# Optimization experiments

Measured on AMD Instinct MI355X. Metric: run time of the kernel, lower is better.

Reference implementation:

```python
import jax, jax.numpy as jnp
import numpy as np

EPS = 1e-5
N_NODES = 50000


def batchnorm(x, gamma, beta):
    # training-mode BatchNorm1d: batch mean, biased variance
    mean = jnp.mean(x, axis=0)
    var = jnp.mean(jnp.square(x - mean), axis=0)
    return (x - mean) * jax.lax.rsqrt(var + EPS) * gamma + beta


def setup_inputs() -> dict:
    key = jax.random.key(0)
    ks = jax.random.split(key, 8)
    N, E, D_IN, D_H, D_OUT = N_NODES, 800000, 128, 128, 128
    feat = jax.random.normal(ks[0], (N, D_IN), dtype=jnp.float32)
    w = jax.random.uniform(ks[1], (E,), dtype=jnp.float32)
    # xavier_uniform with relu gain for Q and W
    gain = float(np.sqrt(2.0))
    bq = gain * np.sqrt(6.0 / (D_IN + D_H))
    bw = gain * np.sqrt(6.0 / (D_IN + D_H + D_OUT))
    Q_w = jax.random.uniform(ks[2], (D_H, D_IN), minval=-bq, maxval=bq, dtype=jnp.float32)
    W_w = jax.random.uniform(ks[3], (D_OUT, D_IN + D_H), minval=-bw, maxval=bw, dtype=jnp.float32)
    Q_b = jnp.zeros((D_H,), jnp.float32)
    W_b = jnp.zeros((D_OUT,), jnp.float32)
    gamma2 = jnp.ones((D_OUT,), jnp.float32)
    beta2 = jnp.zeros((D_OUT,), jnp.float32)
    src = jax.random.randint(ks[4], (E,), 0, N, dtype=jnp.int32)
    dst = jax.random.randint(ks[5], (E,), 0, N, dtype=jnp.int32)
    return {"feat": feat, "w": w, "Q_w": Q_w, "Q_b": Q_b, "W_w": W_w,
            "W_b": W_b, "gamma2": gamma2, "beta2": beta2, "src": src, "dst": dst}


def reference(feat, w, Q_w, Q_b, W_w, W_b, gamma2, beta2, src, dst):
    N = feat.shape[0]
    # h = dropout(bnorm_two(relu(Q(feat))))  (dropout=0 -> identity; source reuses bnorm_two)
    h = batchnorm(jax.nn.relu(feat @ Q_w.T + Q_b), gamma2, beta2)  # [N, H]
    # weighted neighbor mean: sum_e w_e * h[src_e] scattered to dst, / sum_e w_e
    num = jax.ops.segment_sum(w[:, None] * h[src], dst, num_segments=N)  # [N, H]
    den = jax.ops.segment_sum(w, dst, num_segments=N)  # [N]
    has_msg = den[:, None] != 0
    agg = jnp.where(has_msg, num / jnp.where(has_msg, den[:, None], 1.0), h)
    rst = jnp.concatenate([feat, agg], axis=1) @ W_w.T + W_b  # [N, OUT]
    rst = batchnorm(jax.nn.relu(rst), gamma2, beta2)
    denom = jnp.linalg.norm(rst, axis=1, keepdims=True)
    return rst / jnp.where(denom == 0, 1.0, denom)
```

## Files before the change

### kernel.cpp

```cpp
#include <hip/hip_runtime.h>
#include <stdint.h>


#define BN_EPS 1e-5f
#define NSLOT 32

typedef __attribute__((ext_vector_type(8))) short bf16x8;
typedef __attribute__((ext_vector_type(4))) float f32x4;

static __device__ __forceinline__ unsigned short f2bf(float f) {
    uint32_t u = __builtin_bit_cast(uint32_t, f);
    u += 0x7fffu + ((u >> 16) & 1u);
    return (unsigned short)(u >> 16);
}
static __device__ __forceinline__ float bf_lo(uint32_t u) {
    return __builtin_bit_cast(float, u << 16);
}
static __device__ __forceinline__ float bf_hi(uint32_t u) {
    return __builtin_bit_cast(float, u & 0xffff0000u);
}

__global__ __launch_bounds__(256) void k_pre(
    const float* __restrict__ feat, unsigned short* __restrict__ featb, int nf,
    const int* __restrict__ dst, int* __restrict__ cnt, int E, int CB)
{
    if ((int)blockIdx.x < CB) {
        int i = (blockIdx.x * 256 + threadIdx.x) * 4;
        if (i + 3 < nf) {
            float4 v = *(const float4*)(feat + i);
            ushort4 o;
            o.x = f2bf(v.x); o.y = f2bf(v.y); o.z = f2bf(v.z); o.w = f2bf(v.w);
            *(ushort4*)(featb + i) = o;
        } else {
            for (int j = i; j < nf; ++j) featb[j] = f2bf(feat[j]);
        }
    } else {
        int e = (blockIdx.x - CB) * 256 + threadIdx.x;
        if (e < E) atomicAdd(&cnt[dst[e]], 1);
    }
}

__global__ __launch_bounds__(1024) void k_scan_part(
    const int* __restrict__ cnt, int* __restrict__ offs,
    int* __restrict__ bsum)
{
    __shared__ int wsum[16];
    const int tid = threadIdx.x, lane = tid & 63, wv = tid >> 6;
    const int i = blockIdx.x * 4096 + tid * 4;
    int4 v = *(const int4*)(cnt + i);
    int s = v.x + v.y + v.z + v.w;
    int incl = s;
#pragma unroll
    for (int o = 1; o < 64; o <<= 1) {
        int t = __shfl_up(incl, o, 64);
        if (lane >= o) incl += t;
    }
    if (lane == 63) wsum[wv] = incl;
    __syncthreads();
    if (wv == 0 && lane < 16) {
        int t = wsum[lane];
        int ss = t;
#pragma unroll
        for (int o = 1; o < 16; o <<= 1) {
            int u = __shfl_up(ss, o, 64);
            if (lane >= o) ss += u;
        }
        wsum[lane] = ss - t;
        if (lane == 15 && bsum) bsum[blockIdx.x] = ss;
    }
    __syncthreads();
    int e0 = wsum[wv] + incl - s;
    int4 o;
    o.x = e0; o.y = e0 + v.x; o.z = o.y + v.y; o.w = o.z + v.z;
    *(int4*)(offs + i) = o;
}

__global__ __launch_bounds__(1024) void k_scan_fix(
    int* __restrict__ offs, const int* __restrict__ bsum,
    int* __restrict__ gcur, int N, int E)
{
    __shared__ int pre_s;
    const int tid = threadIdx.x;
    if (tid == 0) {
        int p = 0;
        for (int j = 0; j < (int)blockIdx.x; ++j) p += bsum[j];
        pre_s = p;
    }
    __syncthreads();
    const int pre = pre_s;
    const int i = blockIdx.x * 4096 + tid * 4;
    int4 v = *(const int4*)(offs + i);
    v.x += pre; v.y += pre; v.z += pre; v.w += pre;
    if (i + 3 < N) {
        *(int4*)(offs + i) = v;
    } else {
        int vv[4] = {v.x, v.y, v.z, v.w};
        for (int j = 0; j < 4; ++j) {
            int idx = i + j;
            if (idx < N) offs[idx] = vv[j];
            else if (idx == N) offs[idx] = E;
        }
    }
    if ((tid & 127) == 0 && i < N) gcur[i >> 9] = v.x;
}

template<int K>
__global__ __launch_bounds__(256) void gemm_bn(
    const unsigned short* __restrict__ A_lo,
    const unsigned short* __restrict__ A_hi,
    const float* __restrict__ B,
    const float* __restrict__ bias,
    float* __restrict__ Y,
    double* __restrict__ sum, double* __restrict__ sumsq, int N)
{
    constexpr int SA = 72;
    __shared__ unsigned short As[64 * SA];
    __shared__ unsigned short Bs[128 * SA];
    __shared__ float bsum_s[128], bsq_s[128];

    const int tid  = threadIdx.x;
    const int lane = tid & 63;
    const int wv   = tid >> 6;
    const int wr   = wv >> 1;
    const int wc   = wv & 1;
    const int m15  = lane & 15;
    const int quad = lane >> 4;
    const int r0   = blockIdx.x * 64;

    if (tid < 128) { bsum_s[tid] = 0.f; bsq_s[tid] = 0.f; }

    f32x4 acc[2][4];
#pragma unroll
    for (int rt = 0; rt < 2; ++rt)
#pragma unroll
        for (int ct = 0; ct < 4; ++ct)
            acc[rt][ct] = (f32x4){0.f, 0.f, 0.f, 0.f};

    for (int kc = 0; kc < K; kc += 64) {
        const unsigned short* Ap = (kc < 128) ? A_lo : A_hi;
        const int koff = kc & 127;
#pragma unroll
        for (int i = 0; i < 2; ++i) {
            int idx = i * 256 + tid;
            int row = idx >> 3, seg = idx & 7;
            int gr  = r0 + row; if (gr >= N) gr = N - 1;
            uint4 v = *(const uint4*)(Ap + (size_t)gr * 128 + koff + seg * 8);
            *(uint4*)(As + row * SA + seg * 8) = v;
        }
#pragma unroll
        for (int i = 0; i < 8; ++i) {
            int idx = i * 256 + tid;
            int row = idx >> 4, seg = idx & 15;
            float4 v = *(const float4*)(B + (size_t)row * K + kc + seg * 4);
            ushort4 o;
            o.x = f2bf(v.x); o.y = f2bf(v.y); o.z = f2bf(v.z); o.w = f2bf(v.w);
            *(ushort4*)(Bs + row * SA + seg * 4) = o;
        }
        __syncthreads();

#pragma unroll
        for (int ks = 0; ks < 64; ks += 32) {
            bf16x8 af[2], bfr[4];
#pragma unroll
            for (int rt = 0; rt < 2; ++rt)
                af[rt] = *(const bf16x8*)(As + (wr * 32 + rt * 16 + m15) * SA + ks + quad * 8);
#pragma unroll
            for (int ct = 0; ct < 4; ++ct)
                bfr[ct] = *(const bf16x8*)(Bs + (wc * 64 + ct * 16 + m15) * SA + ks + quad * 8);
#pragma unroll
            for (int rt = 0; rt < 2; ++rt)
#pragma unroll
                for (int ct = 0; ct < 4; ++ct)
                    acc[rt][ct] = __builtin_amdgcn_mfma_f32_16x16x32_bf16(
                        af[rt], bfr[ct], acc[rt][ct], 0, 0, 0);
        }
        __syncthreads();
    }

#pragma unroll
    for (int ct = 0; ct < 4; ++ct) {
        int col = wc * 64 + ct * 16 + m15;
        float bz = bias[col];
        float s = 0.f, q = 0.f;
#pragma unroll
        for (int rt = 0; rt < 2; ++rt) {
#pragma unroll
            for (int reg = 0; reg < 4; ++reg) {
                int row = r0 + wr * 32 + rt * 16 + quad * 4 + reg;
                float v = fmaxf(acc[rt][ct][reg] + bz, 0.f);
                if (row < N) {
                    Y[(size_t)row * 128 + col] = v;
                } else {
                    v = 0.f;
                }
                s += v; q = fmaf(v, v, q);
            }
        }
        s += __shfl_xor(s, 16, 64); s += __shfl_xor(s, 32, 64);
        q += __shfl_xor(q, 16, 64); q += __shfl_xor(q, 32, 64);
        if (quad == 0) {
            atomicAdd(&bsum_s[col], s);
            atomicAdd(&bsq_s[col], q);
        }
    }
    __syncthreads();
    if (tid < 128) {
        const int slot = (blockIdx.x & (NSLOT - 1)) * 128;
        atomicAdd(&sum[slot + tid],   (double)bsum_s[tid]);
        atomicAdd(&sumsq[slot + tid], (double)bsq_s[tid]);
    }
}

__global__ __launch_bounds__(128) void bn_coef(
    const double* __restrict__ sum, const double* __restrict__ sumsq,
    const float* __restrict__ gamma, const float* __restrict__ beta,
    float* __restrict__ a, float* __restrict__ b, double invN)
{
    const int t = threadIdx.x;
    double ms = 0.0, qs = 0.0;
#pragma unroll
    for (int s = 0; s < NSLOT; ++s) {
        ms += sum[s * 128 + t];
        qs += sumsq[s * 128 + t];
    }
    float mean = (float)(ms * invN);
    float var  = (float)(qs * invN) - mean * mean;
    float sc = rsqrtf(var + BN_EPS) * gamma[t];
    a[t] = sc;
    b[t] = fmaf(-mean, sc, beta[t]);
}

__global__ __launch_bounds__(256) void apply_bn_bf16(
    const float* __restrict__ y,
    const float* __restrict__ a, const float* __restrict__ b,
    unsigned short* __restrict__ h, int n)
{
    int i = (blockIdx.x * 256 + threadIdx.x) * 4;
    if (i >= n) return;
    int c = i & 127;
    float4 v  = *(const float4*)(y + i);
    float4 av = *(const float4*)(a + c);
    float4 bv = *(const float4*)(b + c);
    ushort4 o;
    o.x = f2bf(fmaf(av.x, v.x, bv.x));
    o.y = f2bf(fmaf(av.y, v.y, bv.y));
    o.z = f2bf(fmaf(av.z, v.z, bv.z));
    o.w = f2bf(fmaf(av.w, v.w, bv.w));
    *(ushort4*)(h + i) = o;
}

__global__ __launch_bounds__(256) void k_bin(
    const int* __restrict__ src, const int* __restrict__ dst,
    const float* __restrict__ w, int* __restrict__ gcur,
    int4* __restrict__ tmp, int E)
{
    __shared__ int hcnt[128];
    __shared__ int hbase[128];
    const int tid = threadIdx.x;
    if (tid < 128) hcnt[tid] = 0;
    __syncthreads();

    int d8[8], s8[8], slot8[8];
    float w8[8];
#pragma unroll
    for (int j = 0; j < 8; ++j) {
        int e = blockIdx.x * 2048 + j * 256 + tid;
        if (e < E) {
            d8[j] = dst[e]; s8[j] = src[e]; w8[j] = w[e];
            slot8[j] = atomicAdd(&hcnt[d8[j] >> 9], 1);
        } else d8[j] = -1;
    }
    __syncthreads();
    if (tid < 128 && hcnt[tid] > 0)
        hbase[tid] = atomicAdd(&gcur[tid], hcnt[tid]);
    __syncthreads();
#pragma unroll
    for (int j = 0; j < 8; ++j) {
        if (d8[j] >= 0) {
            int pos = hbase[d8[j] >> 9] + slot8[j];
            tmp[pos] = make_int4(s8[j], __float_as_int(w8[j]), d8[j], 0);
        }
    }
}

__global__ __launch_bounds__(256) void k_refine(
    const int4* __restrict__ tmp, const int* __restrict__ offs,
    int2* __restrict__ epack, int N)
{
    __shared__ int lcur[512];
    const int b    = blockIdx.x;
    const int d0   = b << 9;
    const int dlim = min(512, N - d0);
    for (int i = threadIdx.x; i < dlim; i += 256) lcur[i] = offs[d0 + i];
    __syncthreads();
    const int start = offs[d0];
    const int end   = offs[d0 + dlim];
    for (int p = start + threadIdx.x; p < end; p += 256) {
        int4 rec = tmp[p];
        int pos = atomicAdd(&lcur[rec.z - d0], 1);
        epack[pos] = make_int2(rec.x, rec.y);
    }
}

__global__ __launch_bounds__(256) void gather_agg(
    const unsigned short* __restrict__ h,
    const int* __restrict__ offs, const int2* __restrict__ epack,
    unsigned short* __restrict__ aggb, int N)
{
    const int r    = (int)((blockIdx.x * 256u + threadIdx.x) >> 6);
    const int lane = threadIdx.x & 63;
    if (r >= N) return;
    int p = offs[r];
    const int end = offs[r + 1];
    float nx = 0.f, ny = 0.f, den = 0.f;
    for (; p + 3 < end; p += 4) {
        int2 e0 = epack[p],     e1 = epack[p + 1];
        int2 e2 = epack[p + 2], e3 = epack[p + 3];
        uint32_t u0 = *(const uint32_t*)(h + (size_t)e0.x * 128 + 2 * lane);
        uint32_t u1 = *(const uint32_t*)(h + (size_t)e1.x * 128 + 2 * lane);
        uint32_t u2 = *(const uint32_t*)(h + (size_t)e2.x * 128 + 2 * lane);
        uint32_t u3 = *(const uint32_t*)(h + (size_t)e3.x * 128 + 2 * lane);
        float w0 = __int_as_float(e0.y), w1 = __int_as_float(e1.y);
        float w2 = __int_as_float(e2.y), w3 = __int_as_float(e3.y);
        nx = fmaf(w0, bf_lo(u0), nx); ny = fmaf(w0, bf_hi(u0), ny);
        nx = fmaf(w1, bf_lo(u1), nx); ny = fmaf(w1, bf_hi(u1), ny);
        nx = fmaf(w2, bf_lo(u2), nx); ny = fmaf(w2, bf_hi(u2), ny);
        nx = fmaf(w3, bf_lo(u3), nx); ny = fmaf(w3, bf_hi(u3), ny);
        den += (w0 + w1) + (w2 + w3);
    }
    for (; p < end; ++p) {
        int2 e0 = epack[p];
        float w0 = __int_as_float(e0.y);
        uint32_t u0 = *(const uint32_t*)(h + (size_t)e0.x * 128 + 2 * lane);
        nx = fmaf(w0, bf_lo(u0), nx); ny = fmaf(w0, bf_hi(u0), ny);
        den += w0;
    }
    float2 outv;
    if (den != 0.f) {
        float inv = 1.f / den;
        outv.x = nx * inv; outv.y = ny * inv;
    } else {
        uint32_t u = *(const uint32_t*)(h + (size_t)r * 128 + 2 * lane);
        outv.x = bf_lo(u); outv.y = bf_hi(u);
    }
    ushort2 ao; ao.x = f2bf(outv.x); ao.y = f2bf(outv.y);
    *(ushort2*)&aggb[(size_t)r * 128 + 2 * lane] = ao;
}

__global__ __launch_bounds__(256) void finalize(
    const float* __restrict__ Y2,
    const float* __restrict__ a, const float* __restrict__ b,
    float* __restrict__ out, int N)
{
    __shared__ float sa[128], sb[128];
    const int t = threadIdx.x;
    if (t < 128) { sa[t] = a[t]; sb[t] = b[t]; }
    __syncthreads();
    const int row  = (int)((blockIdx.x * 256u + t) >> 6);
    const int lane = t & 63;
    if (row >= N) return;
    const size_t base = (size_t)row * 128;
    float v0 = fmaf(sa[lane],      Y2[base + lane],      sb[lane]);
    float v1 = fmaf(sa[lane + 64], Y2[base + lane + 64], sb[lane + 64]);
    float ss = fmaf(v0, v0, v1 * v1);
#pragma unroll
    for (int o = 32; o; o >>= 1) ss += __shfl_xor(ss, o, 64);
    float nrm = sqrtf(ss);
    float inv = (nrm == 0.f) ? 1.f : 1.f / nrm;
    out[base + lane]      = v0 * inv;
    out[base + lane + 64] = v1 * inv;
}

extern "C" void kernel_launch(void* const* d_in, const int* in_sizes, int n_in,
                              void* d_out, int out_size, void* d_ws, size_t ws_size,
                              hipStream_t stream)
{
    const float* feat   = (const float*)d_in[0];
    const float* w      = (const float*)d_in[1];
    const float* Q_w    = (const float*)d_in[2];
    const float* Q_b    = (const float*)d_in[3];
    const float* W_w    = (const float*)d_in[4];
    const float* W_b    = (const float*)d_in[5];
    const float* gamma2 = (const float*)d_in[6];
    const float* beta2  = (const float*)d_in[7];
    const int*   src    = (const int*)d_in[8];
    const int*   dst    = (const int*)d_in[9];

    const int N = in_sizes[0] / 128;
    const int E = in_sizes[1];

    const int SB = (N + 4095) / 4096;
    const int NP = SB * 4096;

    float*          y1    = (float*)d_ws;
    unsigned short* featb = (unsigned short*)(y1 + (size_t)N * 128);
    unsigned short* aggb  = featb + (size_t)N * 128;
    unsigned short* h_bf  = aggb + (size_t)N * 128;
    int4*  tmp    = (int4*)(h_bf + (size_t)N * 128);
    int2*  epack  = (int2*)(tmp + E);
    int*   offs   = (int*)(epack + E);
    int*   gcur   = offs + NP + 4;
    int*   bsum   = gcur + 128;
    float* coefs  = (float*)(bsum + 16);
    float* a1 = coefs, *b1 = coefs + 128, *a2 = coefs + 256, *b2 = coefs + 384;
    double* stats = (double*)(coefs + 512);
    double* sum1   = stats;
    double* sumsq1 = stats + NSLOT * 128;
    double* sum2   = stats + 2 * NSLOT * 128;
    double* sumsq2 = stats + 3 * NSLOT * 128;
    int*   cnt    = (int*)(stats + 4 * NSLOT * 128);

    hipMemsetAsync(stats, 0,
                   4 * NSLOT * 128 * sizeof(double) + (size_t)NP * sizeof(int),
                   stream);

    const double invN = 1.0 / (double)N;
    const int gemm_blocks = (N + 63) / 64;
    const int NB = (N + 511) >> 9;
    const int CB = (N * 128 / 4 + 255) / 256;

    k_pre<<<CB + (E + 255) / 256, 256, 0, stream>>>(
        feat, featb, N * 128, dst, cnt, E, CB);
    k_scan_part<<<SB, 1024, 0, stream>>>(cnt, offs, bsum);
    k_scan_fix<<<SB, 1024, 0, stream>>>(offs, bsum, gcur, N, E);

    k_bin<<<(E + 2047) / 2048, 256, 0, stream>>>(src, dst, w, gcur, tmp, E);
    k_refine<<<NB, 256, 0, stream>>>(tmp, offs, epack, N);

    gemm_bn<128><<<gemm_blocks, 256, 0, stream>>>(
        featb, featb, Q_w, Q_b, y1, sum1, sumsq1, N);
    bn_coef<<<1, 128, 0, stream>>>(sum1, sumsq1, gamma2, beta2, a1, b1, invN);
    apply_bn_bf16<<<(N * 128 + 1023) / 1024, 256, 0, stream>>>(
        y1, a1, b1, h_bf, N * 128);

    gather_agg<<<(N * 64 + 255) / 256, 256, 0, stream>>>(h_bf, offs, epack, aggb, N);

    gemm_bn<256><<<gemm_blocks, 256, 0, stream>>>(
        featb, aggb, W_w, W_b, y1 , sum2, sumsq2, N);
    bn_coef<<<1, 128, 0, stream>>>(sum2, sumsq2, gamma2, beta2, a2, b2, invN);
    finalize<<<(N * 64 + 255) / 256, 256, 0, stream>>>(
        y1, a2, b2, (float*)d_out, N);
}
```

Measured before the change: 265.8 us.

## Replace per-node count and global scan with coarse bucket histogram and per-bucket local scan

Counting now happens per 512-node bucket, using a shared-memory histogram and only 128 global atomics per block, instead of one global atomic per edge into a per-node count array. The two-kernel global prefix scan over per-node counts is replaced by a single tiny 128-entry scan. Per-node offsets are then computed inside k_refine with a local histogram and scan. This removes a kernel launch, the large count memset and many contended global atomics, at the cost of k_refine reading tmp twice.

```diff
diff --git a/kernel.cpp b/kernel.cpp
--- a/kernel.cpp
+++ b/kernel.cpp
@@ -22,7 +22,7 @@
 
 __global__ __launch_bounds__(256) void k_pre(
     const float* __restrict__ feat, unsigned short* __restrict__ featb, int nf,
-    const int* __restrict__ dst, int* __restrict__ cnt, int E, int CB)
+    const int* __restrict__ dst, int* __restrict__ ccnt, int E, int CB)
 {
     if ((int)blockIdx.x < CB) {
         int i = (blockIdx.x * 256 + threadIdx.x) * 4;
@@ -35,73 +35,41 @@
             for (int j = i; j < nf; ++j) featb[j] = f2bf(feat[j]);
         }
     } else {
-        int e = (blockIdx.x - CB) * 256 + threadIdx.x;
-        if (e < E) atomicAdd(&cnt[dst[e]], 1);
-    }
-}
-
-__global__ __launch_bounds__(1024) void k_scan_part(
-    const int* __restrict__ cnt, int* __restrict__ offs,
-    int* __restrict__ bsum)
-{
-    __shared__ int wsum[16];
-    const int tid = threadIdx.x, lane = tid & 63, wv = tid >> 6;
-    const int i = blockIdx.x * 4096 + tid * 4;
-    int4 v = *(const int4*)(cnt + i);
-    int s = v.x + v.y + v.z + v.w;
-    int incl = s;
+        __shared__ int hcnt[128];
+        const int tid = threadIdx.x;
+        if (tid < 128) hcnt[tid] = 0;
+        __syncthreads();
+        const int base_e = (blockIdx.x - CB) * 2048;
+#pragma unroll
+        for (int j = 0; j < 8; ++j) {
+            int e = base_e + j * 256 + tid;
+            if (e < E) atomicAdd(&hcnt[dst[e] >> 9], 1);
+        }
+        __syncthreads();
+        if (tid < 128 && hcnt[tid] > 0) atomicAdd(&ccnt[tid], hcnt[tid]);
+    }
+}
+
+__global__ __launch_bounds__(128) void k_coffs(
+    const int* __restrict__ ccnt, int* __restrict__ coffs,
+    int* __restrict__ gcur, int* __restrict__ offs, int N, int E)
+{
+    __shared__ int w0sum;
+    const int t = threadIdx.x;
+    const int lane = t & 63, wv = t >> 6;
+    int v = ccnt[t];
+    int incl = v;
 #pragma unroll
     for (int o = 1; o < 64; o <<= 1) {
-        int t = __shfl_up(incl, o, 64);
-        if (lane >= o) incl += t;
-    }
-    if (lane == 63) wsum[wv] = incl;
-    __syncthreads();
-    if (wv == 0 && lane < 16) {
-        int t = wsum[lane];
-        int ss = t;
-#pragma unroll
-        for (int o = 1; o < 16; o <<= 1) {
-            int u = __shfl_up(ss, o, 64);
-            if (lane >= o) ss += u;
-        }
-        wsum[lane] = ss - t;
-        if (lane == 15 && bsum) bsum[blockIdx.x] = ss;
-    }
-    __syncthreads();
-    int e0 = wsum[wv] + incl - s;
-    int4 o;
-    o.x = e0; o.y = e0 + v.x; o.z = o.y + v.y; o.w = o.z + v.z;
-    *(int4*)(offs + i) = o;
-}
-
-__global__ __launch_bounds__(1024) void k_scan_fix(
-    int* __restrict__ offs, const int* __restrict__ bsum,
-    int* __restrict__ gcur, int N, int E)
-{
-    __shared__ int pre_s;
-    const int tid = threadIdx.x;
-    if (tid == 0) {
-        int p = 0;
-        for (int j = 0; j < (int)blockIdx.x; ++j) p += bsum[j];
-        pre_s = p;
-    }
-    __syncthreads();
-    const int pre = pre_s;
-    const int i = blockIdx.x * 4096 + tid * 4;
-    int4 v = *(const int4*)(offs + i);
-    v.x += pre; v.y += pre; v.z += pre; v.w += pre;
-    if (i + 3 < N) {
-        *(int4*)(offs + i) = v;
-    } else {
-        int vv[4] = {v.x, v.y, v.z, v.w};
-        for (int j = 0; j < 4; ++j) {
-            int idx = i + j;
-            if (idx < N) offs[idx] = vv[j];
-            else if (idx == N) offs[idx] = E;
-        }
-    }
-    if ((tid & 127) == 0 && i < N) gcur[i >> 9] = v.x;
+        int u = __shfl_up(incl, o, 64);
+        if (lane >= o) incl += u;
+    }
+    if (wv == 0 && lane == 63) w0sum = incl;
+    __syncthreads();
+    int excl = incl - v + (wv ? w0sum : 0);
+    coffs[t] = excl;
+    gcur[t]  = excl;
+    if (t == 127) { coffs[128] = excl + v; offs[N] = E; }
 }
 
 template<int K>
@@ -284,20 +252,52 @@
 }
 
 __global__ __launch_bounds__(256) void k_refine(
-    const int4* __restrict__ tmp, const int* __restrict__ offs,
-    int2* __restrict__ epack, int N)
-{
-    __shared__ int lcur[512];
+    const int4* __restrict__ tmp, const int* __restrict__ coffs,
+    int* __restrict__ offs, int2* __restrict__ epack, int N)
+{
+    __shared__ int hist[512];
+    __shared__ int wpre[4];
     const int b    = blockIdx.x;
     const int d0   = b << 9;
     const int dlim = min(512, N - d0);
-    for (int i = threadIdx.x; i < dlim; i += 256) lcur[i] = offs[d0 + i];
-    __syncthreads();
-    const int start = offs[d0];
-    const int end   = offs[d0 + dlim];
-    for (int p = start + threadIdx.x; p < end; p += 256) {
+    const int tid  = threadIdx.x;
+    const int lane = tid & 63, wv = tid >> 6;
+    const int start = coffs[b];
+    const int end   = coffs[b + 1];
+
+    hist[tid] = 0; hist[tid + 256] = 0;
+    __syncthreads();
+
+    for (int p = start + tid; p < end; p += 256)
+        atomicAdd(&hist[tmp[p].z - d0], 1);
+    __syncthreads();
+
+    int v0 = hist[2 * tid], v1 = hist[2 * tid + 1];
+    int s = v0 + v1;
+    int incl = s;
+#pragma unroll
+    for (int o = 1; o < 64; o <<= 1) {
+        int t = __shfl_up(incl, o, 64);
+        if (lane >= o) incl += t;
+    }
+    if (lane == 63) wpre[wv] = incl;
+    __syncthreads();
+    if (tid == 0) {
+        int r = 0;
+#pragma unroll
+        for (int i = 0; i < 4; ++i) { int t = wpre[i]; wpre[i] = r; r += t; }
+    }
+    __syncthreads();
+    int e0 = start + wpre[wv] + incl - s;
+    if (2 * tid < dlim)     offs[d0 + 2 * tid]     = e0;
+    if (2 * tid + 1 < dlim) offs[d0 + 2 * tid + 1] = e0 + v0;
+    hist[2 * tid]     = e0;
+    hist[2 * tid + 1] = e0 + v0;
+    __syncthreads();
+
+    for (int p = start + tid; p < end; p += 256) {
         int4 rec = tmp[p];
-        int pos = atomicAdd(&lcur[rec.z - d0], 1);
+        int pos = atomicAdd(&hist[rec.z - d0], 1);
         epack[pos] = make_int2(rec.x, rec.y);
     }
 }
@@ -389,9 +389,6 @@
     const int N = in_sizes[0] / 128;
     const int E = in_sizes[1];
 
-    const int SB = (N + 4095) / 4096;
-    const int NP = SB * 4096;
-
     float*          y1    = (float*)d_ws;
     unsigned short* featb = (unsigned short*)(y1 + (size_t)N * 128);
     unsigned short* aggb  = featb + (size_t)N * 128;
@@ -399,33 +396,33 @@
     int4*  tmp    = (int4*)(h_bf + (size_t)N * 128);
     int2*  epack  = (int2*)(tmp + E);
     int*   offs   = (int*)(epack + E);
-    int*   gcur   = offs + NP + 4;
-    int*   bsum   = gcur + 128;
-    float* coefs  = (float*)(bsum + 16);
+    int*   coffs  = offs + (N + 1);
+    int*   gcur   = coffs + 129;
+    float* coefs  = (float*)(gcur + 128);
     float* a1 = coefs, *b1 = coefs + 128, *a2 = coefs + 256, *b2 = coefs + 384;
-    double* stats = (double*)(coefs + 512);
+    uintptr_t sp  = ((uintptr_t)(coefs + 512) + 7) & ~(uintptr_t)7;
+    double* stats = (double*)sp;
     double* sum1   = stats;
     double* sumsq1 = stats + NSLOT * 128;
     double* sum2   = stats + 2 * NSLOT * 128;
     double* sumsq2 = stats + 3 * NSLOT * 128;
-    int*   cnt    = (int*)(stats + 4 * NSLOT * 128);
+    int*   ccnt   = (int*)(stats + 4 * NSLOT * 128);
 
     hipMemsetAsync(stats, 0,
-                   4 * NSLOT * 128 * sizeof(double) + (size_t)NP * sizeof(int),
+                   4 * NSLOT * 128 * sizeof(double) + 128 * sizeof(int),
                    stream);
 
     const double invN = 1.0 / (double)N;
     const int gemm_blocks = (N + 63) / 64;
     const int NB = (N + 511) >> 9;
     const int CB = (N * 128 / 4 + 255) / 256;
-
-    k_pre<<<CB + (E + 255) / 256, 256, 0, stream>>>(
-        feat, featb, N * 128, dst, cnt, E, CB);
-    k_scan_part<<<SB, 1024, 0, stream>>>(cnt, offs, bsum);
-    k_scan_fix<<<SB, 1024, 0, stream>>>(offs, bsum, gcur, N, E);
-
-    k_bin<<<(E + 2047) / 2048, 256, 0, stream>>>(src, dst, w, gcur, tmp, E);
-    k_refine<<<NB, 256, 0, stream>>>(tmp, offs, epack, N);
+    const int HB = (E + 2047) / 2048;
+
+    k_pre<<<CB + HB, 256, 0, stream>>>(feat, featb, N * 128, dst, ccnt, E, CB);
+    k_coffs<<<1, 128, 0, stream>>>(ccnt, coffs, gcur, offs, N, E);
+
+    k_bin<<<HB, 256, 0, stream>>>(src, dst, w, gcur, tmp, E);
+    k_refine<<<NB, 256, 0, stream>>>(tmp, coffs, offs, epack, N);
 
     gemm_bn<128><<<gemm_blocks, 256, 0, stream>>>(
         featb, featb, Q_w, Q_b, y1, sum1, sumsq1, N);
```

After: 254.3 us. 4.3% less time.
